# Optimization experiments

Measured on AMD Instinct MI355X. Metric: run time of the kernel, lower is better.

## Reference

```python
import jax, jax.numpy as jnp
import numpy as np

N_NODES, N_EDGES, B = 100000, 200000, 2048
ND, ED, HID, OUT, HEADS = 64, 16, 512, 512, 4

# dummy-graph topology: central node 0 -> features 1..6, plus self loops (GATv2 default)
D_SRC = jnp.array([0, 0, 0, 0, 0, 0, 0, 1, 2, 3, 4, 5, 6])
D_DST = jnp.array([1, 2, 3, 4, 5, 6, 0, 1, 2, 3, 4, 5, 6])


def setup_inputs() -> dict:
    key = jax.random.key(0)
    ks = jax.random.split(key, 40)
    p = lambda k, sh: (jax.random.normal(k, sh, dtype=jnp.float32) * 0.05)
    inp = {
        'x': jax.random.normal(ks[0], (N_NODES, ND), dtype=jnp.float32),
        'edge_index': jax.random.randint(ks[1], (2, N_EDGES), 0, N_NODES),
        'edge_attr': jax.random.normal(ks[2], (N_EDGES, ED), dtype=jnp.float32),
        'batch': jnp.sort(jax.random.randint(ks[3], (N_NODES,), 0, B)),
        'ecfp': jax.random.uniform(ks[4], (B, OUT), dtype=jnp.float32),
        'topo': jax.random.uniform(ks[5], (B, OUT), dtype=jnp.float32),
        'maccs': jax.random.uniform(ks[6], (B, OUT), dtype=jnp.float32),
        'estate': jax.random.uniform(ks[7], (B, OUT), dtype=jnp.float32),
        'rdkit2d': jax.random.normal(ks[8], (B, OUT), dtype=jnp.float32),
        'phar2d': jax.random.normal(ks[9], (B, OUT), dtype=jnp.float32),
        # GINEConv 1: nn = Linear(ND, HID); edge proj Linear(ED, ND)
        'g1_W': p(ks[10], (ND, HID)), 'g1_b': p(ks[11], (HID,)),
        'e1_W': p(ks[12], (ED, ND)), 'e1_b': p(ks[13], (ND,)),
        'bn1_g': jnp.ones((HID,), jnp.float32), 'bn1_b': jnp.zeros((HID,), jnp.float32),
        # GINEConv 2: nn = Linear(HID, OUT); edge proj Linear(ED, HID)
        'g2_W': p(ks[14], (HID, OUT)), 'g2_b': p(ks[15], (OUT,)),
        'e2_W': p(ks[16], (ED, HID)), 'e2_b': p(ks[17], (HID,)),
        'bn2_g': jnp.ones((OUT,), jnp.float32), 'bn2_b': jnp.zeros((OUT,), jnp.float32),
        # GATv2Conv 1: OUT -> HID, heads, concat=False
        'gat1_Wl': p(ks[18], (OUT, HEADS * HID)), 'gat1_bl': p(ks[19], (HEADS * HID,)),
        'gat1_Wr': p(ks[20], (OUT, HEADS * HID)), 'gat1_br': p(ks[21], (HEADS * HID,)),
        'gat1_att': p(ks[22], (HEADS, HID)), 'gat1_bias': p(ks[23], (HID,)),
        'bn3_g': jnp.ones((HID,), jnp.float32), 'bn3_b': jnp.zeros((HID,), jnp.float32),
        # GATv2Conv 2: HID -> HID
        'gat2_Wl': p(ks[24], (HID, HEADS * HID)), 'gat2_bl': p(ks[25], (HEADS * HID,)),
        'gat2_Wr': p(ks[26], (HID, HEADS * HID)), 'gat2_br': p(ks[27], (HEADS * HID,)),
        'gat2_att': p(ks[28], (HEADS, HID)), 'gat2_bias': p(ks[29], (HID,)),
        'bn4_g': jnp.ones((HID,), jnp.float32), 'bn4_b': jnp.zeros((HID,), jnp.float32),
        'fc_W': p(ks[30], (HID, 1)), 'fc_b': p(ks[31], (1,)),
    }
    return inp


def _bn_eval(h, g, b):
    # PyG BatchNorm in eval mode with fresh running stats (mean=0, var=1)
    return g * (h * (1.0 / np.sqrt(1.0 + 1e-5))) + b


def _gatv2(z, Wl, bl, Wr, br, att, bias):
    # z: [B, 7, Cin]; GATv2Conv with self-loops, concat=False (mean over heads)
    Bn, Nn, _ = z.shape
    Hh, Co = att.shape
    gl = (z @ Wl + bl).reshape(Bn, Nn, Hh, Co)  # source transform
    gr = (z @ Wr + br).reshape(Bn, Nn, Hh, Co)  # target transform
    e = jax.nn.leaky_relu(gl[:, D_SRC] + gr[:, D_DST], 0.2)  # [B, 13, H, Co]
    logits = jnp.einsum('behc,hc->beh', e, att)  # [B, 13, H]

    def seg_softmax(lg):
        m = jax.ops.segment_max(lg, D_DST, num_segments=7)
        ex = jnp.exp(lg - m[D_DST])
        s = jax.ops.segment_sum(ex, D_DST, num_segments=7)
        return ex / s[D_DST]

    alpha = jax.vmap(seg_softmax)(logits)  # [B, 13, H]
    msg = gl[:, D_SRC] * alpha[..., None]  # [B, 13, H, Co]
    out = jax.vmap(lambda mm: jax.ops.segment_sum(mm, D_DST, num_segments=7))(msg)
    return out.mean(axis=2) + bias  # [B, 7, Co]


def reference(x, edge_index, edge_attr, batch, ecfp, topo, maccs, estate, rdkit2d, phar2d,
              g1_W, g1_b, e1_W, e1_b, bn1_g, bn1_b,
              g2_W, g2_b, e2_W, e2_b, bn2_g, bn2_b,
              gat1_Wl, gat1_bl, gat1_Wr, gat1_br, gat1_att, gat1_bias, bn3_g, bn3_b,
              gat2_Wl, gat2_bl, gat2_Wr, gat2_br, gat2_att, gat2_bias, bn4_g, bn4_b,
              fc_W, fc_b):
    N = x.shape[0]
    Bg = ecfp.shape[0]
    src, dst = edge_index[0], edge_index[1]
    # GINEConv 1: msg = relu(x_j + W_e e), sum-aggr, out = Lin(x + aggr) (eps=0)
    m = jax.nn.relu(x[src] + (edge_attr @ e1_W + e1_b))
    h = (x + jax.ops.segment_sum(m, dst, num_segments=N)) @ g1_W + g1_b
    h = jax.nn.relu(_bn_eval(h, bn1_g, bn1_b))  # dropout = identity (eval)
    # GINEConv 2
    m2 = jax.nn.relu(h[src] + (edge_attr @ e2_W + e2_b))
    h2 = (h + jax.ops.segment_sum(m2, dst, num_segments=N)) @ g2_W + g2_b
    h2 = jax.nn.relu(_bn_eval(h2, bn2_g, bn2_b))
    # global mean pool
    sums = jax.ops.segment_sum(h2, batch, num_segments=Bg)
    cnts = jax.ops.segment_sum(jnp.ones((N,), h2.dtype), batch, num_segments=Bg)
    graph_out = sums / jnp.maximum(cnts, 1.0)[:, None]  # [B, OUT]
    # batched 7-node dummy graphs (node 0 = graph embedding, 1..6 = features)
    xn = jnp.stack([graph_out, ecfp, topo, maccs, estate, rdkit2d, phar2d], axis=1)
    z = _gatv2(xn, gat1_Wl, gat1_bl, gat1_Wr, gat1_br, gat1_att, gat1_bias)
    z = jax.nn.relu(_bn_eval(z, bn3_g, bn3_b))
    z = _gatv2(z, gat2_Wl, gat2_bl, gat2_Wr, gat2_br, gat2_att, gat2_bias)
    z = jax.nn.relu(_bn_eval(z, bn4_g, bn4_b))
    return z[:, 0, :] @ fc_W + fc_b  # [B, 1]
```

## Files before the change

### kernel.cpp

```cpp
#include <hip/hip_runtime.h>
#include <hip/hip_bf16.h>

#define N_NODESC 100000
#define N_EDGESC 200000
#define BG 2048
#define NDIM 64
#define EDIM 16

typedef __bf16 bf16x8 __attribute__((ext_vector_type(8)));
typedef float f32x4 __attribute__((ext_vector_type(4)));

static __device__ __forceinline__ float bn_inv() { return 0.9999950000374997f; }

__global__ void zero_f4(float4* __restrict__ p, int n4) {
    int i = blockIdx.x * 256 + threadIdx.x;
    if (i < n4) p[i] = make_float4(0.f, 0.f, 0.f, 0.f);
}
__global__ void zero_int(int* __restrict__ p, int n) {
    int i = blockIdx.x * 256 + threadIdx.x;
    if (i < n) p[i] = 0;
}
__global__ void zero_out(float* __restrict__ p, int n) {
    int i = blockIdx.x * 256 + threadIdx.x;
    if (i < n) p[i] = 0.f;
}

__global__ void hist_dst(const int* __restrict__ dst, int* __restrict__ deg) {
    int i = blockIdx.x * 256 + threadIdx.x;
    if (i < N_EDGESC) atomicAdd(&deg[dst[i]], 1);
}
__global__ void scan_bsums(const int* __restrict__ deg, int* __restrict__ bsum, int n) {
    __shared__ int ls[256];
    int b = blockIdx.x, t = threadIdx.x;
    int s = 0;
#pragma unroll
    for (int j = 0; j < 4; j++) {
        int i = b * 1024 + t * 4 + j;
        if (i < n) s += deg[i];
    }
    ls[t] = s;
    __syncthreads();
    for (int off = 128; off; off >>= 1) {
        if (t < off) ls[t] += ls[t + off];
        __syncthreads();
    }
    if (t == 0) bsum[b] = ls[0];
}
__global__ void scan_top(int* __restrict__ bsum, int nb, int* __restrict__ total) {
    if (threadIdx.x == 0) {
        int acc = 0;
        for (int i = 0; i < nb; i++) { int v = bsum[i]; bsum[i] = acc; acc += v; }
        *total = acc;
    }
}
__global__ void scan_final(const int* __restrict__ deg, const int* __restrict__ bsum,
                           int* __restrict__ rowptr, int* __restrict__ cursor, int n) {
    __shared__ int ls[256];
    int b = blockIdx.x, t = threadIdx.x;
    int v[4], s = 0;
#pragma unroll
    for (int j = 0; j < 4; j++) {
        int i = b * 1024 + t * 4 + j;
        v[j] = (i < n) ? deg[i] : 0;
        s += v[j];
    }
    ls[t] = s;
    __syncthreads();
    int run = s;
    for (int off = 1; off < 256; off <<= 1) {
        int add = (t >= off) ? ls[t - off] : 0;
        __syncthreads();
        ls[t] += add;
        __syncthreads();
    }
    int excl = ls[t] - run + bsum[b];
#pragma unroll
    for (int j = 0; j < 4; j++) {
        int i = b * 1024 + t * 4 + j;
        if (i < n) { rowptr[i] = excl; cursor[i] = excl; excl += v[j]; }
    }
}
__global__ void scatter_eid(const int* __restrict__ dst, int* __restrict__ cursor,
                            int* __restrict__ eid) {
    int e = blockIdx.x * 256 + threadIdx.x;
    if (e < N_EDGESC) {
        int p = atomicAdd(&cursor[dst[e]], 1);
        eid[p] = e;
    }
}

__global__ void transpose_w(const float* __restrict__ W, __hip_bfloat16* __restrict__ hi,
                            int K, int N) {
    __shared__ float t[64][65];
    int k0 = blockIdx.x * 64, n0 = blockIdx.y * 64;
    int tid = threadIdx.x, tx = tid & 63, ty = tid >> 6;
    for (int r = ty; r < 64; r += 4) t[r][tx] = W[(size_t)(k0 + r) * N + n0 + tx];
    __syncthreads();
    for (int r = ty; r < 64; r += 4)
        hi[(size_t)(n0 + r) * K + k0 + tx] = __float2bfloat16(t[tx][r]);
}

__global__ void concat_bias(const float* __restrict__ a, const float* __restrict__ b,
                            float* __restrict__ o) {
    int i = blockIdx.x * 256 + threadIdx.x;
    if (i < 2048) { o[i] = a[i]; o[2048 + i] = b[i]; }
}

#define G1_NPW 8
__global__ __launch_bounds__(256, 2) void gine1_gather(
    const float* __restrict__ x, const int* __restrict__ srcv, const float* __restrict__ ea,
    const float* __restrict__ e1W, const float* __restrict__ e1b,
    const int* __restrict__ rowptr, const int* __restrict__ eid,
    __hip_bfloat16* __restrict__ xin) {
    int tid = threadIdx.x;
    int wave = tid >> 6, lane = tid & 63;
    float wreg[16];
#pragma unroll
    for (int k = 0; k < 16; k++) wreg[k] = e1W[k * 64 + lane];
    float bb = e1b[lane];
    int nbase = (blockIdx.x * 4 + wave) * G1_NPW;
#pragma unroll 1
    for (int it = 0; it < G1_NPW; it++) {
        int n = nbase + it;
        if (n >= N_NODESC) return;
        float acc = x[(size_t)n * 64 + lane];
        int beg = rowptr[n], end = rowptr[n + 1];
        for (int idx = beg; idx < end; idx++) {
            int e = eid[idx], s = srcv[e];
            const float4* ef = (const float4*)(ea + (size_t)e * 16);
            float4 e0 = ef[0], e1 = ef[1], e2 = ef[2], e3 = ef[3];
            float p = bb;
            p = fmaf(e0.x, wreg[0], p);  p = fmaf(e0.y, wreg[1], p);
            p = fmaf(e0.z, wreg[2], p);  p = fmaf(e0.w, wreg[3], p);
            p = fmaf(e1.x, wreg[4], p);  p = fmaf(e1.y, wreg[5], p);
            p = fmaf(e1.z, wreg[6], p);  p = fmaf(e1.w, wreg[7], p);
            p = fmaf(e2.x, wreg[8], p);  p = fmaf(e2.y, wreg[9], p);
            p = fmaf(e2.z, wreg[10], p); p = fmaf(e2.w, wreg[11], p);
            p = fmaf(e3.x, wreg[12], p); p = fmaf(e3.y, wreg[13], p);
            p = fmaf(e3.z, wreg[14], p); p = fmaf(e3.w, wreg[15], p);
            acc += fmaxf(x[(size_t)s * 64 + lane] + p, 0.f);
        }
        xin[(size_t)n * 64 + lane] = __float2bfloat16(acc);
    }
}

#define G2_NPB 16
__global__ __launch_bounds__(256, 2) void gine2_gather(
    const __hip_bfloat16* __restrict__ h, const int* __restrict__ srcv,
    const float* __restrict__ ea, const float* __restrict__ e2W,
    const float* __restrict__ e2b, const int* __restrict__ rowptr,
    const int* __restrict__ eid, __hip_bfloat16* __restrict__ a2, int n0, int n1) {
    int tid = threadIdx.x;
    int half = tid >> 7, lt = tid & 127;
    float wreg[4][16], breg[4];
#pragma unroll
    for (int j = 0; j < 4; j++) {
        int c = lt * 4 + j;
        breg[j] = e2b[c];
#pragma unroll
        for (int k = 0; k < 16; k++) wreg[j][k] = e2W[k * 512 + c];
    }
    int nbase = n0 + blockIdx.x * G2_NPB + half;
#pragma unroll 1
    for (int it = 0; it < G2_NPB / 2; it++) {
        int n = nbase + it * 2;
        if (n >= n1) return;
        short4 hv = *(const short4*)((const short*)(h + (size_t)n * 512) + lt * 4);
        const __hip_bfloat16* hb = (const __hip_bfloat16*)&hv;
        float acc[4];
#pragma unroll
        for (int j = 0; j < 4; j++) acc[j] = __bfloat162float(hb[j]);
        int beg = rowptr[n], end = rowptr[n + 1];
        for (int idx = beg; idx < end; idx++) {
            int e = eid[idx], s = srcv[e];
            const float4* ef = (const float4*)(ea + (size_t)e * 16);
            float4 e0 = ef[0], e1 = ef[1], e2v = ef[2], e3 = ef[3];
            short4 sv = *(const short4*)((const short*)(h + (size_t)s * 512) + lt * 4);
            const __hip_bfloat16* sb = (const __hip_bfloat16*)&sv;
#pragma unroll
            for (int j = 0; j < 4; j++) {
                float p = breg[j];
                p = fmaf(e0.x, wreg[j][0], p);  p = fmaf(e0.y, wreg[j][1], p);
                p = fmaf(e0.z, wreg[j][2], p);  p = fmaf(e0.w, wreg[j][3], p);
                p = fmaf(e1.x, wreg[j][4], p);  p = fmaf(e1.y, wreg[j][5], p);
                p = fmaf(e1.z, wreg[j][6], p);  p = fmaf(e1.w, wreg[j][7], p);
                p = fmaf(e2v.x, wreg[j][8], p); p = fmaf(e2v.y, wreg[j][9], p);
                p = fmaf(e2v.z, wreg[j][10], p);p = fmaf(e2v.w, wreg[j][11], p);
                p = fmaf(e3.x, wreg[j][12], p); p = fmaf(e3.y, wreg[j][13], p);
                p = fmaf(e3.z, wreg[j][14], p); p = fmaf(e3.w, wreg[j][15], p);
                acc[j] += fmaxf(__bfloat162float(sb[j]) + p, 0.f);
            }
        }
        __hip_bfloat16 o[4];
#pragma unroll
        for (int j = 0; j < 4; j++) o[j] = __float2bfloat16(acc[j]);
        *(short4*)((short*)(a2 + (size_t)(n - n0) * 512) + lt * 4) = *(const short4*)o;
    }
}

#define ASTR 40
template <int MODE>
__global__ __launch_bounds__(256, 2) void mfma_gemm(
    const __hip_bfloat16* __restrict__ A, const __hip_bfloat16* __restrict__ Bhi,
    int M, int K, int N, const float* __restrict__ bias, const float* __restrict__ bng,
    const float* __restrict__ bnb, const int* __restrict__ batch,
    float* __restrict__ psum, __hip_bfloat16* __restrict__ Cout) {
    __shared__ short As[128 * ASTR];
    __shared__ short Bh[128 * ASTR];
    int r0 = blockIdx.y * 128;
    int n0 = blockIdx.x * 128;
    int tid = threadIdx.x;
    int lane = tid & 63;
    int wm = ((tid >> 6) >> 1) * 64, wn = ((tid >> 6) & 1) * 64;

    f32x4 acc[4][4];
#pragma unroll
    for (int i = 0; i < 4; i++)
#pragma unroll
        for (int j = 0; j < 4; j++) acc[i][j] = (f32x4){0.f, 0.f, 0.f, 0.f};

    for (int k0 = 0; k0 < K; k0 += 32) {
        __syncthreads();
#pragma unroll
        for (int j = 0; j < 2; j++) {
            int i = tid + j * 256;
            int row = i >> 2, cb = i & 3;
            int grow = r0 + row;
            if (grow >= M) grow = M - 1;
            *(int4*)(As + row * ASTR + cb * 8) =
                *(const int4*)(A + (size_t)grow * K + k0 + cb * 8);
        }
#pragma unroll
        for (int j = 0; j < 2; j++) {
            int i = tid + j * 256;
            int row = i >> 2, cb = i & 3;
            *(int4*)(Bh + row * ASTR + cb * 8) =
                *(const int4*)(Bhi + (size_t)(n0 + row) * K + k0 + cb * 8);
        }
        __syncthreads();
        int fi = lane & 15, kb = (lane >> 4) * 8;
        bf16x8 af[4], bhf[4];
#pragma unroll
        for (int mi = 0; mi < 4; mi++)
            af[mi] = *(const bf16x8*)(As + (wm + mi * 16 + fi) * ASTR + kb);
#pragma unroll
        for (int ni = 0; ni < 4; ni++)
            bhf[ni] = *(const bf16x8*)(Bh + (wn + ni * 16 + fi) * ASTR + kb);
#pragma unroll
        for (int mi = 0; mi < 4; mi++)
#pragma unroll
            for (int ni = 0; ni < 4; ni++)
                acc[mi][ni] = __builtin_amdgcn_mfma_f32_16x16x32_bf16(af[mi], bhf[ni],
                                                                     acc[mi][ni], 0, 0, 0);
    }
    int col_l = lane & 15, quad = lane >> 4;
#pragma unroll
    for (int mi = 0; mi < 4; mi++) {
        int rbase = r0 + wm + mi * 16 + quad * 4;
#pragma unroll
        for (int ni = 0; ni < 4; ni++) {
            int gcol = n0 + wn + ni * 16 + col_l;
            if (MODE == 0) {
                float b0 = bias[gcol];
#pragma unroll
                for (int reg = 0; reg < 4; reg++) {
                    int grow = rbase + reg;
                    if (grow < M)
                        Cout[(size_t)grow * N + gcol] = __float2bfloat16(acc[mi][ni][reg] + b0);
                }
            } else {
                float b0 = bias[gcol], g0 = bng[gcol], bb0 = bnb[gcol];
                float vv[4];
#pragma unroll
                for (int reg = 0; reg < 4; reg++)
                    vv[reg] = fmaxf(fmaf((acc[mi][ni][reg] + b0) * bn_inv(), g0, bb0), 0.f);
                if (MODE == 1) {
#pragma unroll
                    for (int reg = 0; reg < 4; reg++) {
                        int grow = rbase + reg;
                        if (grow < M) Cout[(size_t)grow * 512 + gcol] = __float2bfloat16(vv[reg]);
                    }
                } else {
                    if (rbase + 3 < M && batch[rbase] == batch[rbase + 3]) {
                        atomicAdd(&psum[(size_t)batch[rbase] * 512 + gcol],
                                  (vv[0] + vv[1]) + (vv[2] + vv[3]));
                    } else {
#pragma unroll
                        for (int reg = 0; reg < 4; reg++) {
                            int grow = rbase + reg;
                            if (grow < M)
                                atomicAdd(&psum[(size_t)batch[grow] * 512 + gcol], vv[reg]);
                        }
                    }
                }
            }
        }
    }
}

__global__ void count_nodes(const int* __restrict__ batch, float* __restrict__ cnt) {
    int i = blockIdx.x * 256 + threadIdx.x;
    if (i < N_NODESC) atomicAdd(&cnt[batch[i]], 1.0f);
}

__global__ void build_xn(const float* __restrict__ psum, const float* __restrict__ cnt,
                         const float* __restrict__ ecfp, const float* __restrict__ topo,
                         const float* __restrict__ maccs, const float* __restrict__ estate,
                         const float* __restrict__ rdkit2d, const float* __restrict__ phar2d,
                         __hip_bfloat16* __restrict__ xn) {
    int i = blockIdx.x * 256 + threadIdx.x;
    if (i >= BG * 512) return;
    int bidx = i >> 9, c = i & 511;
    float cv = fmaxf(cnt[bidx], 1.0f);
    __hip_bfloat16* o = xn + (size_t)bidx * 7 * 512;
    o[c] = __float2bfloat16(psum[i] / cv);
    o[512 + c] = __float2bfloat16(ecfp[i]);
    o[2 * 512 + c] = __float2bfloat16(topo[i]);
    o[3 * 512 + c] = __float2bfloat16(maccs[i]);
    o[4 * 512 + c] = __float2bfloat16(estate[i]);
    o[5 * 512 + c] = __float2bfloat16(rdkit2d[i]);
    o[6 * 512 + c] = __float2bfloat16(phar2d[i]);
}

__global__ void gat_attn(const __hip_bfloat16* __restrict__ cg,
                         const float* __restrict__ att, const float* __restrict__ bias,
                         const float* __restrict__ bng, const float* __restrict__ bnb,
                         __hip_bfloat16* __restrict__ zout) {
    int b = blockIdx.x;
    int tid = threadIdx.x;
    int wave = tid >> 6, lane = tid & 63;
    __shared__ float logits[13][4];
    __shared__ float alpha[13][4];
    const size_t base = (size_t)b * 7 * 4096;
    for (int p = wave; p < 52; p += 4) {
        int e = p >> 2, hh = p & 3;
        int se = (e < 7) ? 0 : (e - 6);
        int de = (e < 6) ? (e + 1) : ((e == 6) ? 0 : (e - 6));
        const __hip_bfloat16* glp = cg + base + (size_t)se * 4096 + hh * 512;
        const __hip_bfloat16* grp = cg + base + (size_t)de * 4096 + 2048 + hh * 512;
        const float* ap = att + hh * 512;
        float s = 0.f;
#pragma unroll
        for (int j = 0; j < 8; j++) {
            int c = lane + j * 64;
            float v = __bfloat162float(glp[c]) + __bfloat162float(grp[c]);
            v = (v >= 0.f) ? v : 0.2f * v;
            s = fmaf(v, ap[c], s);
        }
#pragma unroll
        for (int off = 32; off; off >>= 1) s += __shfl_down(s, off);
        if (lane == 0) logits[e][hh] = s;
    }
    __syncthreads();
    if (tid < 24) {
        int n = 1 + (tid >> 2), hh = tid & 3;
        float la = logits[n - 1][hh], lb = logits[6 + n][hh];
        float m = fmaxf(la, lb);
        float ea = __expf(la - m), eb = __expf(lb - m);
        float inv = 1.f / (ea + eb);
        alpha[n - 1][hh] = ea * inv;
        alpha[6 + n][hh] = eb * inv;
    } else if (tid < 28) {
        alpha[6][tid & 3] = 1.f;
    }
    __syncthreads();
    for (int i = tid; i < 7 * 512; i += 256) {
        int n = i >> 9, c = i & 511;
        float v = 0.f;
        if (n == 0) {
#pragma unroll
            for (int hh = 0; hh < 4; hh++)
                v = fmaf(alpha[6][hh],
                         __bfloat162float(cg[base + (size_t)hh * 512 + c]), v);
        } else {
#pragma unroll
            for (int hh = 0; hh < 4; hh++) {
                v = fmaf(alpha[n - 1][hh],
                         __bfloat162float(cg[base + (size_t)hh * 512 + c]), v);
                v = fmaf(alpha[6 + n][hh],
                         __bfloat162float(cg[base + (size_t)n * 4096 + hh * 512 + c]), v);
            }
        }
        v = fmaf(v, 0.25f, bias[c]);
        v = fmaf(v * bn_inv(), bng[c], bnb[c]);
        zout[(size_t)b * 7 * 512 + i] = __float2bfloat16(fmaxf(v, 0.f));
    }
}

__global__ void final_fc(const __hip_bfloat16* __restrict__ z, const float* __restrict__ fcW,
                         const float* __restrict__ fcb, float* __restrict__ out) {
    int b = blockIdx.x * 4 + (threadIdx.x >> 6);
    int lane = threadIdx.x & 63;
    if (b >= BG) return;
    const __hip_bfloat16* row = z + (size_t)b * 7 * 512;
    float s = 0.f;
#pragma unroll
    for (int j = 0; j < 8; j++)
        s = fmaf(__bfloat162float(row[lane + j * 64]), fcW[lane + j * 64], s);
#pragma unroll
    for (int off = 32; off; off >>= 1) s += __shfl_down(s, off);
    if (lane == 0) out[b] = s + fcb[0];
}

extern "C" void kernel_launch(void* const* d_in, const int* in_sizes, int n_in,
                              void* d_out, int out_size, void* d_ws, size_t ws_size,
                              hipStream_t stream) {
    const float* x = (const float*)d_in[0];
    const int* eidx = (const int*)d_in[1];
    const float* eattr = (const float*)d_in[2];
    const int* batch = (const int*)d_in[3];
    const float* ecfp = (const float*)d_in[4];
    const float* topo = (const float*)d_in[5];
    const float* maccs = (const float*)d_in[6];
    const float* estate = (const float*)d_in[7];
    const float* rdkit2d = (const float*)d_in[8];
    const float* phar2d = (const float*)d_in[9];
    const float* g1_W = (const float*)d_in[10];
    const float* g1_b = (const float*)d_in[11];
    const float* e1_W = (const float*)d_in[12];
    const float* e1_b = (const float*)d_in[13];
    const float* bn1_g = (const float*)d_in[14];
    const float* bn1_b = (const float*)d_in[15];
    const float* g2_W = (const float*)d_in[16];
    const float* g2_b = (const float*)d_in[17];
    const float* e2_W = (const float*)d_in[18];
    const float* e2_b = (const float*)d_in[19];
    const float* bn2_g = (const float*)d_in[20];
    const float* bn2_b = (const float*)d_in[21];
    const float* gat1_Wl = (const float*)d_in[22];
    const float* gat1_bl = (const float*)d_in[23];
    const float* gat1_Wr = (const float*)d_in[24];
    const float* gat1_br = (const float*)d_in[25];
    const float* gat1_att = (const float*)d_in[26];
    const float* gat1_bias = (const float*)d_in[27];
    const float* bn3_g = (const float*)d_in[28];
    const float* bn3_b = (const float*)d_in[29];
    const float* gat2_Wl = (const float*)d_in[30];
    const float* gat2_bl = (const float*)d_in[31];
    const float* gat2_Wr = (const float*)d_in[32];
    const float* gat2_br = (const float*)d_in[33];
    const float* gat2_att = (const float*)d_in[34];
    const float* gat2_bias = (const float*)d_in[35];
    const float* bn4_g = (const float*)d_in[36];
    const float* bn4_b = (const float*)d_in[37];
    const float* fc_W = (const float*)d_in[38];
    const float* fc_b = (const float*)d_in[39];
    float* out = (float*)d_out;

    const size_t NEEDED = 194682880ull;
    if (ws_size < NEEDED) {
        zero_out<<<(BG + 255) / 256, 256, 0, stream>>>(out, BG);
        return;
    }
    char* w = (char*)d_ws;
    __hip_bfloat16* H = (__hip_bfloat16*)w;
    __hip_bfloat16* CG = (__hip_bfloat16*)w;
    __hip_bfloat16* A2 = (__hip_bfloat16*)(w + 102400000);
    __hip_bfloat16* GW12 = (__hip_bfloat16*)(w + 117440512);
    __hip_bfloat16* GW34 = (__hip_bfloat16*)(w + 121634816);
    __hip_bfloat16* Z1B = (__hip_bfloat16*)(w + 125829120);
    float* B12 = (float*)(w + 140509184);
    float* B34 = (float*)(w + 140525568);

    char* C = w + 161120256;
    __hip_bfloat16* XIN = (__hip_bfloat16*)C;
    __hip_bfloat16* XNB = (__hip_bfloat16*)C;
    __hip_bfloat16* Z2B = (__hip_bfloat16*)(C + 14680064);
    int* ROWPTR = (int*)(C + 14680064);
    int* CURSOR = (int*)(C + 15080192);
    int* EID = (int*)(C + 15480320);
    int* DEG = (int*)(C + 16280320);
    __hip_bfloat16* G1W = (__hip_bfloat16*)(C + 16680320);
    __hip_bfloat16* G2W = (__hip_bfloat16*)(C + 16745856);
    int* BSUM = (int*)(C + 17270144);

    float* PS = (float*)(w + 190480384);
    float* PC = (float*)(w + 194674688);

    const int* src = eidx;
    const int* dst = eidx + N_EDGESC;

    zero_int<<<(N_NODESC + 255) / 256, 256, 0, stream>>>(DEG, N_NODESC);
    zero_f4<<<(BG * 512 / 4 + 255) / 256, 256, 0, stream>>>((float4*)PS, BG * 512 / 4);
    zero_f4<<<(BG / 4 + 255) / 256, 256, 0, stream>>>((float4*)PC, BG / 4);
    hist_dst<<<(N_EDGESC + 255) / 256, 256, 0, stream>>>(dst, DEG);
    const int NB = (N_NODESC + 1023) / 1024;
    scan_bsums<<<NB, 256, 0, stream>>>(DEG, BSUM, N_NODESC);
    scan_top<<<1, 64, 0, stream>>>(BSUM, NB, ROWPTR + N_NODESC);
    scan_final<<<NB, 256, 0, stream>>>(DEG, BSUM, ROWPTR, CURSOR, N_NODESC);
    scatter_eid<<<(N_EDGESC + 255) / 256, 256, 0, stream>>>(dst, CURSOR, EID);

    transpose_w<<<dim3(1, 8), 256, 0, stream>>>(g1_W, G1W, 64, 512);
    transpose_w<<<dim3(8, 8), 256, 0, stream>>>(g2_W, G2W, 512, 512);

    gine1_gather<<<(N_NODESC + 4 * G1_NPW - 1) / (4 * G1_NPW), 256, 0, stream>>>(
        x, src, eattr, e1_W, e1_b, ROWPTR, EID, XIN);
    mfma_gemm<1><<<dim3(4, (N_NODESC + 127) / 128), 256, 0, stream>>>(
        XIN, G1W, N_NODESC, 64, 512, g1_b, bn1_g, bn1_b, nullptr, nullptr, H);
    count_nodes<<<(N_NODESC + 255) / 256, 256, 0, stream>>>(batch, PC);

    for (int c0n = 0; c0n < N_NODESC; c0n += 50000) {
        int c1n = c0n + 50000;
        int rows = 50000;
        gine2_gather<<<(rows + G2_NPB - 1) / G2_NPB, 256, 0, stream>>>(
            H, src, eattr, e2_W, e2_b, ROWPTR, EID, A2, c0n, c1n);
        mfma_gemm<2><<<dim3(4, (rows + 127) / 128), 256, 0, stream>>>(
            A2, G2W, rows, 512, 512, g2_b, bn2_g, bn2_b, batch + c0n, PS, nullptr);
    }

    transpose_w<<<dim3(8, 32), 256, 0, stream>>>(gat1_Wl, GW12, 512, 2048);
    transpose_w<<<dim3(8, 32), 256, 0, stream>>>(gat1_Wr, GW12 + (size_t)2048 * 512, 512, 2048);
    transpose_w<<<dim3(8, 32), 256, 0, stream>>>(gat2_Wl, GW34, 512, 2048);
    transpose_w<<<dim3(8, 32), 256, 0, stream>>>(gat2_Wr, GW34 + (size_t)2048 * 512, 512, 2048);
    concat_bias<<<8, 256, 0, stream>>>(gat1_bl, gat1_br, B12);
    concat_bias<<<8, 256, 0, stream>>>(gat2_bl, gat2_br, B34);

    build_xn<<<(BG * 512) / 256, 256, 0, stream>>>(PS, PC, ecfp, topo, maccs, estate,
                                                   rdkit2d, phar2d, XNB);
    const int MGAT = BG * 7;
    dim3 ggrid(4096 / 128, MGAT / 128);
    mfma_gemm<0><<<ggrid, 256, 0, stream>>>(XNB, GW12, MGAT, 512, 4096, B12,
                                            nullptr, nullptr, nullptr, nullptr, CG);
    gat_attn<<<BG, 256, 0, stream>>>(CG, gat1_att, gat1_bias, bn3_g, bn3_b, Z1B);
    mfma_gemm<0><<<ggrid, 256, 0, stream>>>(Z1B, GW34, MGAT, 512, 4096, B34,
                                            nullptr, nullptr, nullptr, nullptr, CG);
    gat_attn<<<BG, 256, 0, stream>>>(CG, gat2_att, gat2_bias, bn4_g, bn4_b, Z2B);
    final_fc<<<BG / 4, 256, 0, stream>>>(Z2B, fc_W, fc_b, out);
}
```

Before: 1.052 ms.

## Load MFMA GEMM fragments directly from global memory with register double-buffering

Removes the LDS staging and both __syncthreads from the GEMM main loop. Each wave now loads its A and B MFMA fragments straight from global memory into registers, with a two-stage register prefetch across 64-wide K steps. This is meant to cut barrier and LDS traffic overhead and overlap loads with MFMA work. In exchange, data is no longer shared between waves, so global/L2 traffic rises (each A row is loaded by two waves and each B row by two waves), the per-lane 16-byte loads are strided by rows, and register pressure goes up. The loop also assumes K is a multiple of 64.

```diff
diff --git a/kernel.cpp b/kernel.cpp
--- a/kernel.cpp
+++ b/kernel.cpp
@@ -198,20 +198,19 @@
     }
 }
 
-#define ASTR 40
 template <int MODE>
 __global__ __launch_bounds__(256, 2) void mfma_gemm(
     const __hip_bfloat16* __restrict__ A, const __hip_bfloat16* __restrict__ Bhi,
     int M, int K, int N, const float* __restrict__ bias, const float* __restrict__ bng,
     const float* __restrict__ bnb, const int* __restrict__ batch,
     float* __restrict__ psum, __hip_bfloat16* __restrict__ Cout) {
-    __shared__ short As[128 * ASTR];
-    __shared__ short Bh[128 * ASTR];
     int r0 = blockIdx.y * 128;
     int n0 = blockIdx.x * 128;
     int tid = threadIdx.x;
     int lane = tid & 63;
-    int wm = ((tid >> 6) >> 1) * 64, wn = ((tid >> 6) & 1) * 64;
+    int wv = tid >> 6;
+    int wm = (wv >> 1) * 64, wn = (wv & 1) * 64;
+    int fi = lane & 15, kb = (lane >> 4) * 8;
 
     f32x4 acc[4][4];
 #pragma unroll
@@ -219,40 +218,50 @@
 #pragma unroll
         for (int j = 0; j < 4; j++) acc[i][j] = (f32x4){0.f, 0.f, 0.f, 0.f};
 
-    for (int k0 = 0; k0 < K; k0 += 32) {
-        __syncthreads();
-#pragma unroll
-        for (int j = 0; j < 2; j++) {
-            int i = tid + j * 256;
-            int row = i >> 2, cb = i & 3;
-            int grow = r0 + row;
-            if (grow >= M) grow = M - 1;
-            *(int4*)(As + row * ASTR + cb * 8) =
-                *(const int4*)(A + (size_t)grow * K + k0 + cb * 8);
+    const __hip_bfloat16* aptr[4];
+    const __hip_bfloat16* bptr[4];
+#pragma unroll
+    for (int mi = 0; mi < 4; mi++) {
+        int grow = r0 + wm + mi * 16 + fi;
+        if (grow >= M) grow = M - 1;
+        aptr[mi] = A + (size_t)grow * K + kb;
+    }
+#pragma unroll
+    for (int ni = 0; ni < 4; ni++)
+        bptr[ni] = Bhi + (size_t)(n0 + wn + ni * 16 + fi) * K + kb;
+
+    bf16x8 ac[4], bc[4], an[4], bn2[4];
+#pragma unroll
+    for (int mi = 0; mi < 4; mi++) ac[mi] = *(const bf16x8*)(aptr[mi]);
+#pragma unroll
+    for (int ni = 0; ni < 4; ni++) bc[ni] = *(const bf16x8*)(bptr[ni]);
+
+#pragma unroll 1
+    for (int k0 = 0; k0 < K; k0 += 64) {
+#pragma unroll
+        for (int mi = 0; mi < 4; mi++) an[mi] = *(const bf16x8*)(aptr[mi] + k0 + 32);
+#pragma unroll
+        for (int ni = 0; ni < 4; ni++) bn2[ni] = *(const bf16x8*)(bptr[ni] + k0 + 32);
+#pragma unroll
+        for (int mi = 0; mi < 4; mi++)
+#pragma unroll
+            for (int ni = 0; ni < 4; ni++)
+                acc[mi][ni] = __builtin_amdgcn_mfma_f32_16x16x32_bf16(ac[mi], bc[ni],
+                                                                     acc[mi][ni], 0, 0, 0);
+        if (k0 + 64 < K) {
+#pragma unroll
+            for (int mi = 0; mi < 4; mi++) ac[mi] = *(const bf16x8*)(aptr[mi] + k0 + 64);
+#pragma unroll
+            for (int ni = 0; ni < 4; ni++) bc[ni] = *(const bf16x8*)(bptr[ni] + k0 + 64);
         }
 #pragma unroll
-        for (int j = 0; j < 2; j++) {
-            int i = tid + j * 256;
-            int row = i >> 2, cb = i & 3;
-            *(int4*)(Bh + row * ASTR + cb * 8) =
-                *(const int4*)(Bhi + (size_t)(n0 + row) * K + k0 + cb * 8);
-        }
-        __syncthreads();
-        int fi = lane & 15, kb = (lane >> 4) * 8;
-        bf16x8 af[4], bhf[4];
-#pragma unroll
         for (int mi = 0; mi < 4; mi++)
-            af[mi] = *(const bf16x8*)(As + (wm + mi * 16 + fi) * ASTR + kb);
-#pragma unroll
-        for (int ni = 0; ni < 4; ni++)
-            bhf[ni] = *(const bf16x8*)(Bh + (wn + ni * 16 + fi) * ASTR + kb);
-#pragma unroll
-        for (int mi = 0; mi < 4; mi++)
 #pragma unroll
             for (int ni = 0; ni < 4; ni++)
-                acc[mi][ni] = __builtin_amdgcn_mfma_f32_16x16x32_bf16(af[mi], bhf[ni],
+                acc[mi][ni] = __builtin_amdgcn_mfma_f32_16x16x32_bf16(an[mi], bn2[ni],
                                                                      acc[mi][ni], 0, 0, 0);
     }
+
     int col_l = lane & 15, quad = lane >> 4;
 #pragma unroll
     for (int mi = 0; mi < 4; mi++) {
```

Measured after the change: 1.398 ms. +32.9%, slower.
